# Optimization experiments

Measured on AMD Instinct MI355X. Metric: run time of the kernel, lower is better.

Reference implementation:

```python
import jax, jax.numpy as jnp
import numpy as np

EMB = 1024
HEADS = 16
HEAD_DIM = EMB // HEADS
D_FF = 4 * EMB
EPS = 1e-5


def setup_inputs() -> dict:
    key = jax.random.key(0)
    ks = jax.random.split(key, 12)
    b, t = 4, 2048
    sc = 0.02
    return {
        "x": jax.random.normal(ks[0], (b, t, EMB), dtype=jnp.float32),
        # weights stored [in, out] (transpose of torch Linear.weight)
        "w_attn": jax.random.normal(ks[1], (EMB, 3 * EMB), dtype=jnp.float32) * sc,
        "b_attn": jnp.zeros((3 * EMB,), dtype=jnp.float32),
        "w_proj": jax.random.normal(ks[2], (EMB, EMB), dtype=jnp.float32) * sc,
        "b_proj": jnp.zeros((EMB,), dtype=jnp.float32),
        "ln1_g": jnp.ones((EMB,), dtype=jnp.float32),
        "ln1_b": jnp.zeros((EMB,), dtype=jnp.float32),
        "w_ff1": jax.random.normal(ks[3], (EMB, D_FF), dtype=jnp.float32) * sc,
        "b_ff1": jnp.zeros((D_FF,), dtype=jnp.float32),
        "w_ff2": jax.random.normal(ks[4], (D_FF, EMB), dtype=jnp.float32) * sc,
        "b_ff2": jnp.zeros((EMB,), dtype=jnp.float32),
        "ln2_g": jnp.ones((EMB,), dtype=jnp.float32),
        "ln2_b": jnp.zeros((EMB,), dtype=jnp.float32),
    }


def _layernorm(x, g, b):
    mu = jnp.mean(x, axis=-1, keepdims=True)
    var = jnp.var(x, axis=-1, keepdims=True)
    return (x - mu) * jax.lax.rsqrt(var + EPS) * g + b


def reference(x, w_attn, b_attn, w_proj, b_proj, ln1_g, ln1_b,
              w_ff1, b_ff1, w_ff2, b_ff2, ln2_g, ln2_b):
    b, t, e = x.shape
    h, s = HEADS, HEAD_DIM
    # fused qkv projection (GPT2-style c_attn)
    qkv = x @ w_attn + b_attn                      # [b, t, 3e]
    q, k, v = jnp.split(qkv, 3, axis=-1)
    q = q.reshape(b, t, h, s).transpose(0, 2, 1, 3)  # [b, h, t, s]
    k = k.reshape(b, t, h, s).transpose(0, 2, 1, 3)
    v = v.reshape(b, t, h, s).transpose(0, 2, 1, 3)
    dot = jnp.einsum('bhqs,bhks->bhqk', q, k) / jnp.sqrt(jnp.float32(s))
    # causal mask: mask_(..., mask_diagonal=False) zeroes i < j (strict upper)
    causal = jnp.tril(jnp.ones((t, t), dtype=bool))
    dot = jnp.where(causal, dot, jnp.float32(-jnp.inf))
    att = jax.nn.softmax(dot, axis=-1)
    out = jnp.einsum('bhqk,bhks->bhqs', att, v)    # [b, h, t, s]
    out = out.transpose(0, 2, 1, 3).reshape(b, t, e)
    attended = out @ w_proj + b_proj
    # residual + LayerNorm (dropout is identity in eval mode)
    x1 = _layernorm(attended + x, ln1_g, ln1_b)
    ff = jax.nn.relu(x1 @ w_ff1 + b_ff1) @ w_ff2 + b_ff2
    return _layernorm(ff + x1, ln2_g, ln2_b)
```

## Files before the change

kernel.cpp:

```cpp
#include <hip/hip_runtime.h>
#include <hip/hip_bf16.h>


typedef __attribute__((ext_vector_type(8))) short bf16x8;
typedef __attribute__((ext_vector_type(4))) float f32x4;

__device__ __forceinline__ unsigned short f2b(float f) {
  unsigned int u = __float_as_uint(f);
  u += 0x7fffu + ((u >> 16) & 1u);
  return (unsigned short)(u >> 16);
}
__device__ __forceinline__ unsigned int pk2b(float a, float b) {
  __hip_bfloat162 h = __float22bfloat162_rn(make_float2(a, b));
  return *(unsigned int*)&h;
}
__device__ __forceinline__ void gload_lds16(const unsigned short* g, unsigned short* l) {
  __builtin_amdgcn_global_load_lds((const __attribute__((address_space(1))) void*)g,
                                   (__attribute__((address_space(3))) void*)l, 16, 0, 0);
}

__global__ __launch_bounds__(256) void cvt_bf16(const float* __restrict__ in,
                                                unsigned short* __restrict__ out, long n) {
  long i = ((long)blockIdx.x * 256 + threadIdx.x) * 4;
  if (i >= n) return;
  float4 v = *(const float4*)(in + i);
  *(ushort4*)(out + i) = make_ushort4(f2b(v.x), f2b(v.y), f2b(v.z), f2b(v.w));
}

__global__ __launch_bounds__(256) void transpose_bf16(const float* __restrict__ in,
                                                      unsigned short* __restrict__ out,
                                                      int R, int C) {
  __shared__ float tile[32][33];
  int c0 = blockIdx.x * 32, r0 = blockIdx.y * 32;
  for (int i = threadIdx.y; i < 32; i += 8)
    tile[i][threadIdx.x] = in[(long)(r0 + i) * C + c0 + threadIdx.x];
  __syncthreads();
  for (int i = threadIdx.y; i < 32; i += 8)
    out[(long)(c0 + i) * R + r0 + threadIdx.x] = f2b(tile[threadIdx.x][i]);
}

template <int EPI>
__global__ __launch_bounds__(512, 2) void gemm256(const unsigned short* __restrict__ A,
                                                  const unsigned short* __restrict__ Bt,
                                                  const float* __restrict__ bias,
                                                  void* __restrict__ Cout,
                                                  void* __restrict__ Cout2,
                                                  int N, int K, int Kstride) {
  __shared__ __align__(16) unsigned short As[4][256 * 32];
  __shared__ __align__(16) unsigned short Bs[4][256 * 32];

  int tid = threadIdx.x;
  int wv = tid >> 6, lane = tid & 63, quad = lane >> 4, l16 = lane & 15;
  int wm = wv >> 2, wn = wv & 3;

  int nwg = gridDim.x, id = blockIdx.x;
  int sid = (id & 7) * (nwg >> 3) + (id >> 3);
  int bm256 = (sid & 31) * 256, bn256 = (sid >> 5) * 256;
  int chunk = blockIdx.y;
  long kbase = (long)chunk * K;

  int row1 = tid >> 2, row2 = row1 + 128;
  long dsl = ((tid & 3) ^ ((tid >> 3) & 3)) * 8;
  const unsigned short* Ap1 = A + (long)(bm256 + row1) * Kstride + kbase + dsl;
  const unsigned short* Ap2 = A + (long)(bm256 + row2) * Kstride + kbase + dsl;
  const unsigned short* Bp1 = Bt + (long)(bn256 + row1) * Kstride + kbase + dsl;
  const unsigned short* Bp2 = Bt + (long)(bn256 + row2) * Kstride + kbase + dsl;
  int ldsoff1 = wv * 512, ldsoff2 = wv * 512 + 4096;

  auto stage = [&](int t) {
    int buf = t & 3;
    long ko = (long)t * 32;
    gload_lds16(Ap1 + ko, &As[buf][ldsoff1]);
    gload_lds16(Ap2 + ko, &As[buf][ldsoff2]);
    gload_lds16(Bp1 + ko, &Bs[buf][ldsoff1]);
    gload_lds16(Bp2 + ko, &Bs[buf][ldsoff2]);
  };

  f32x4 acc[8][4] = {};
  int sl8 = (quad ^ ((l16 >> 1) & 3)) * 8;
  int arow = wm * 128 + l16;
  int brow = wn * 64 + l16;

  int NT = K >> 5;
  stage(0); stage(1); stage(2);
  asm volatile("s_waitcnt vmcnt(8)\n\ts_barrier" ::: "memory");
  __builtin_amdgcn_sched_barrier(0);

  for (int t = 0; t < NT; ++t) {
    if (t + 3 < NT) stage(t + 3);
    __builtin_amdgcn_sched_barrier(0);
    const unsigned short* Ab = &As[t & 3][0];
    const unsigned short* Bb = &Bs[t & 3][0];
    bf16x8 af[8], bfr[4];
#pragma unroll
    for (int i = 0; i < 8; ++i)
      af[i] = *(const bf16x8*)(Ab + (arow + i * 16) * 32 + sl8);
#pragma unroll
    for (int j = 0; j < 4; ++j)
      bfr[j] = *(const bf16x8*)(Bb + (brow + j * 16) * 32 + sl8);
    __builtin_amdgcn_s_setprio(1);
#pragma unroll
    for (int i = 0; i < 8; ++i)
#pragma unroll
      for (int j = 0; j < 4; ++j)
        acc[i][j] = __builtin_amdgcn_mfma_f32_16x16x32_bf16(af[i], bfr[j], acc[i][j], 0, 0, 0);
    __builtin_amdgcn_s_setprio(0);
    __builtin_amdgcn_sched_barrier(0);
    if (t + 1 < NT) {
      if (t + 3 < NT)       asm volatile("s_waitcnt vmcnt(8)\n\ts_barrier" ::: "memory");
      else if (t + 3 == NT) asm volatile("s_waitcnt vmcnt(4)\n\ts_barrier" ::: "memory");
      else                  asm volatile("s_waitcnt vmcnt(0)\n\ts_barrier" ::: "memory");
      __builtin_amdgcn_sched_barrier(0);
    }
  }

  void* Cbase = chunk ? Cout2 : Cout;
#pragma unroll
  for (int i = 0; i < 8; ++i) {
#pragma unroll
    for (int j = 0; j < 4; ++j) {
      int gn = bn256 + wn * 64 + j * 16 + l16;
      float bv = chunk ? 0.f : bias[gn];
      if (EPI == 3 && gn >= 2048) {
        int h = (gn >> 6) & 15, s = gn & 63;
        int gm0 = bm256 + wm * 128 + i * 16 + quad * 4;
        int b = gm0 >> 11, tt0 = gm0 & 2047;
        unsigned short* vt = (unsigned short*)Cout + 16777216L;
        ushort4 us;
        us.x = f2b(acc[i][j][0] + bv);
        us.y = f2b(acc[i][j][1] + bv);
        us.z = f2b(acc[i][j][2] + bv);
        us.w = f2b(acc[i][j][3] + bv);
        *(ushort4*)(vt + (((long)(b * 16 + h)) * 64 + s) * 2048 + tt0) = us;
      } else {
#pragma unroll
        for (int r = 0; r < 4; ++r) {
          int gm = bm256 + wm * 128 + i * 16 + quad * 4 + r;
          float v = acc[i][j][r] + bv;
          if (EPI == 2) v = fmaxf(v, 0.f);
          if (EPI == 0) {
            ((float*)Cbase)[(long)gm * N + gn] = v;
          } else if (EPI == 2) {
            ((unsigned short*)Cbase)[(long)gm * N + gn] = f2b(v);
          } else {
            float sc = (gn < 1024) ? 0.18033688011112042f : 1.0f;
            ((unsigned short*)Cbase)[(long)gm * 2048 + gn] = f2b(v * sc);
          }
        }
      }
    }
  }
}

__global__ __launch_bounds__(256) void attn_mfma(const unsigned short* __restrict__ qkv,
                                                 unsigned short* __restrict__ outp) {
  const int LD = 72;
  __shared__ __align__(16) unsigned short Ks[64 * LD];
  __shared__ __align__(16) unsigned short Vts[64 * LD];
  __shared__ __align__(16) unsigned short Ps[4][16 * LD];
  int qa = blockIdx.x, qb = 31 - qa;
  int h = blockIdx.y, b = blockIdx.z;
  int t = threadIdx.x;
  int w = t >> 6, lane = t & 63, quad = lane >> 4, l16 = lane & 15;
  const unsigned short* qg = qkv + (long)(b * 2048) * 2048 + h * 64;
  const unsigned short* kg = qg + 1024;
  const unsigned short* vg = qkv + 16777216L + (((long)(b * 16 + h)) * 64) * 2048;
  unsigned short* Pw = &Ps[w][0];

  bf16x8 qfa[2], qfb[2];
#pragma unroll
  for (int ks = 0; ks < 2; ++ks) {
    qfa[ks] = *(const bf16x8*)(qg + (long)(qa * 64 + w * 16 + l16) * 2048 + ks * 32 + quad * 8);
    qfb[ks] = *(const bf16x8*)(qg + (long)(qb * 64 + w * 16 + l16) * 2048 + ks * 32 + quad * 8);
  }

  int sr = t >> 2, sc = (t & 3) * 16;
  const unsigned short* kp = kg + (long)sr * 2048 + sc;
  const unsigned short* vp = vg + (long)sr * 2048 + sc;
  int4 kv0 = *(const int4*)kp, kv1 = *(const int4*)(kp + 8);
  int4 vv0 = *(const int4*)vp, vv1 = *(const int4*)(vp + 8);
  kp += (long)64 * 2048;
  vp += 64;

  f32x4 oa[4] = {}, ob[4] = {};
  f32x4 la = {}, lb = {};
  const short ONE = 0x3F80;
  bf16x8 ones = {ONE, ONE, ONE, ONE, ONE, ONE, ONE, ONE};

  auto process = [&](const bf16x8* qf, int qt, int kt, f32x4* oacc, f32x4& lacc) {
    bool diag = (kt == qt);
#pragma unroll
    for (int rg = 0; rg < 4; ++rg) {
      bf16x8 kf0 = *(const bf16x8*)(Ks + (rg * 16 + l16) * LD + quad * 8);
      bf16x8 kf1 = *(const bf16x8*)(Ks + (rg * 16 + l16) * LD + 32 + quad * 8);
      f32x4 st = {};
      st = __builtin_amdgcn_mfma_f32_16x16x32_bf16(kf0, qf[0], st, 0, 0, 0);
      st = __builtin_amdgcn_mfma_f32_16x16x32_bf16(kf1, qf[1], st, 0, 0, 0);
      if (diag) {
        int kq = rg * 16 + quad * 4;
        int qq = w * 16 + l16;
#pragma unroll
        for (int r = 0; r < 4; ++r)
          if (kq + r > qq) st[r] = -1e30f;
      }
      unsigned int lo = pk2b(exp2f(st[0]), exp2f(st[1]));
      unsigned int hi = pk2b(exp2f(st[2]), exp2f(st[3]));
      *(uint2*)(Pw + l16 * LD + rg * 16 + quad * 4) = make_uint2(lo, hi);
    }
#pragma unroll
    for (int kc = 0; kc < 2; ++kc) {
      bf16x8 ap = *(const bf16x8*)(Pw + l16 * LD + kc * 32 + quad * 8);
      lacc = __builtin_amdgcn_mfma_f32_16x16x32_bf16(ap, ones, lacc, 0, 0, 0);
#pragma unroll
      for (int sg = 0; sg < 4; ++sg) {
        bf16x8 vf = *(const bf16x8*)(Vts + (sg * 16 + l16) * LD + kc * 32 + quad * 8);
        oacc[sg] = __builtin_amdgcn_mfma_f32_16x16x32_bf16(ap, vf, oacc[sg], 0, 0, 0);
      }
    }
  };

  for (int kt = 0; kt <= qb; ++kt) {
    __syncthreads();
    *(int4*)(Ks + sr * LD + sc) = kv0;
    *(int4*)(Ks + sr * LD + sc + 8) = kv1;
    *(int4*)(Vts + sr * LD + sc) = vv0;
    *(int4*)(Vts + sr * LD + sc + 8) = vv1;
    __syncthreads();
    if (kt < qb) {
      kv0 = *(const int4*)kp; kv1 = *(const int4*)(kp + 8);
      vv0 = *(const int4*)vp; vv1 = *(const int4*)(vp + 8);
      kp += (long)64 * 2048;
      vp += 64;
    }
    process(qfb, qb, kt, ob, lb);
    if (kt <= qa) process(qfa, qa, kt, oa, la);
  }

  auto epi = [&](int qt, f32x4* oacc, f32x4& lacc) {
#pragma unroll
    for (int r = 0; r < 4; ++r) {
      float invl = 1.f / lacc[r];
      int row = qt * 64 + w * 16 + quad * 4 + r;
      unsigned short* op = outp + ((long)(b * 2048 + row)) * 1024 + h * 64;
#pragma unroll
      for (int sg = 0; sg < 4; ++sg) op[sg * 16 + l16] = f2b(oacc[sg][r] * invl);
    }
  };
  epi(qa, oa, la);
  epi(qb, ob, lb);
}

__global__ __launch_bounds__(256) void ln_kernel(const float* __restrict__ a,
                                                 const float* __restrict__ a2,
                                                 const float* __restrict__ res,
                                                 const float* __restrict__ gam,
                                                 const float* __restrict__ bet,
                                                 float* __restrict__ outf,
                                                 unsigned short* __restrict__ outb) {
  int row = blockIdx.x, t = threadIdx.x;
  float4 av = *(const float4*)(a + (long)row * 1024 + t * 4);
  float4 rv = *(const float4*)(res + (long)row * 1024 + t * 4);
  float v0 = av.x + rv.x, v1 = av.y + rv.y, v2 = av.z + rv.z, v3 = av.w + rv.w;
  if (a2) {
    float4 a2v = *(const float4*)(a2 + (long)row * 1024 + t * 4);
    v0 += a2v.x; v1 += a2v.y; v2 += a2v.z; v3 += a2v.w;
  }
  float s = v0 + v1 + v2 + v3;
  float ss = v0 * v0 + v1 * v1 + v2 * v2 + v3 * v3;
#pragma unroll
  for (int off = 32; off >= 1; off >>= 1) {
    s += __shfl_down(s, off);
    ss += __shfl_down(ss, off);
  }
  __shared__ float sb[4], ssb[4];
  __shared__ float mean_s, inv_s;
  int w = t >> 6, lane = t & 63;
  if (lane == 0) { sb[w] = s; ssb[w] = ss; }
  __syncthreads();
  if (t == 0) {
    float S = sb[0] + sb[1] + sb[2] + sb[3];
    float SS = ssb[0] + ssb[1] + ssb[2] + ssb[3];
    float mean = S * (1.f / 1024.f);
    float var = SS * (1.f / 1024.f) - mean * mean;
    mean_s = mean;
    inv_s = rsqrtf(var + 1e-5f);
  }
  __syncthreads();
  float mean = mean_s, inv = inv_s;
  int c = t * 4;
  float4 gv = *(const float4*)(gam + c);
  float4 bv = *(const float4*)(bet + c);
  float y0 = (v0 - mean) * inv * gv.x + bv.x;
  float y1 = (v1 - mean) * inv * gv.y + bv.y;
  float y2 = (v2 - mean) * inv * gv.z + bv.z;
  float y3 = (v3 - mean) * inv * gv.w + bv.w;
  *(float4*)(outf + (long)row * 1024 + c) = make_float4(y0, y1, y2, y3);
  if (outb) {
    *(ushort4*)(outb + (long)row * 1024 + c) = make_ushort4(f2b(y0), f2b(y1), f2b(y2), f2b(y3));
  }
}

extern "C" void kernel_launch(void* const* d_in, const int* in_sizes, int n_in,
                              void* d_out, int out_size, void* d_ws, size_t ws_size,
                              hipStream_t stream) {
  const float* x      = (const float*)d_in[0];
  const float* w_attn = (const float*)d_in[1];
  const float* b_attn = (const float*)d_in[2];
  const float* w_proj = (const float*)d_in[3];
  const float* b_proj = (const float*)d_in[4];
  const float* ln1_g  = (const float*)d_in[5];
  const float* ln1_b  = (const float*)d_in[6];
  const float* w_ff1  = (const float*)d_in[7];
  const float* b_ff1  = (const float*)d_in[8];
  const float* w_ff2  = (const float*)d_in[9];
  const float* b_ff2  = (const float*)d_in[10];
  const float* ln2_g  = (const float*)d_in[11];
  const float* ln2_b  = (const float*)d_in[12];

  const long M = 8192, E = 1024;
  char* ws = (char*)d_ws;
  unsigned short* xb   = (unsigned short*)ws; ws += M * E * 2;
  unsigned short* wTa  = (unsigned short*)ws; ws += 3072L * 1024 * 2;
  unsigned short* wTp  = (unsigned short*)ws; ws += 1024L * 1024 * 2;
  unsigned short* wTf1 = (unsigned short*)ws; ws += 4096L * 1024 * 2;
  unsigned short* wTf2 = (unsigned short*)ws; ws += 4096L * 1024 * 2;
  unsigned short* qkvb = (unsigned short*)ws; ws += M * 3072 * 2;
  unsigned short* attb = (unsigned short*)ws; ws += M * E * 2;
  float* a1f = (float*)ws; ws += M * E * 4;
  float* x1f = (float*)ws; ws += M * E * 4;
  unsigned short* x1b = (unsigned short*)ws; ws += M * E * 2;
  unsigned short* hb = qkvb;
  float* f2 = a1f;
  float* prj1 = (float*)qkvb;
  float* ff21 = (float*)d_ws;

  cvt_bf16<<<dim3((M * E) / 4 / 256), dim3(256), 0, stream>>>(x, xb, M * E);
  transpose_bf16<<<dim3(3072 / 32, 1024 / 32), dim3(32, 8), 0, stream>>>(w_attn, wTa, 1024, 3072);
  transpose_bf16<<<dim3(1024 / 32, 1024 / 32), dim3(32, 8), 0, stream>>>(w_proj, wTp, 1024, 1024);
  transpose_bf16<<<dim3(4096 / 32, 1024 / 32), dim3(32, 8), 0, stream>>>(w_ff1, wTf1, 1024, 4096);
  transpose_bf16<<<dim3(1024 / 32, 4096 / 32), dim3(32, 8), 0, stream>>>(w_ff2, wTf2, 4096, 1024);
  gemm256<3><<<dim3(384, 1), dim3(512), 0, stream>>>(xb, wTa, b_attn, qkvb, nullptr, 3072, 1024, 1024);
  attn_mfma<<<dim3(16, 16, 4), dim3(256), 0, stream>>>(qkvb, attb);
  gemm256<0><<<dim3(128, 2), dim3(512), 0, stream>>>(attb, wTp, b_proj, a1f, prj1, 1024, 512, 1024);
  ln_kernel<<<dim3(8192), dim3(256), 0, stream>>>(a1f, prj1, x, ln1_g, ln1_b, x1f, x1b);
  gemm256<2><<<dim3(512, 1), dim3(512), 0, stream>>>(x1b, wTf1, b_ff1, hb, nullptr, 4096, 1024, 1024);
  gemm256<0><<<dim3(128, 2), dim3(512), 0, stream>>>(hb, wTf2, b_ff2, f2, ff21, 1024, 2048, 4096);
  ln_kernel<<<dim3(8192), dim3(256), 0, stream>>>(f2, ff21, x1f, ln2_g, ln2_b, (float*)d_out, nullptr);
}
```

Baseline: 602.0 us.

## Split GEMM k-step into two half-phases interleaving A/B prefetch with MFMA

```diff
diff --git a/kernel.cpp b/kernel.cpp
--- a/kernel.cpp
+++ b/kernel.cpp
@@ -65,16 +65,7 @@
   const unsigned short* Ap2 = A + (long)(bm256 + row2) * Kstride + kbase + dsl;
   const unsigned short* Bp1 = Bt + (long)(bn256 + row1) * Kstride + kbase + dsl;
   const unsigned short* Bp2 = Bt + (long)(bn256 + row2) * Kstride + kbase + dsl;
-  int ldsoff1 = wv * 512, ldsoff2 = wv * 512 + 4096;
-
-  auto stage = [&](int t) {
-    int buf = t & 3;
-    long ko = (long)t * 32;
-    gload_lds16(Ap1 + ko, &As[buf][ldsoff1]);
-    gload_lds16(Ap2 + ko, &As[buf][ldsoff2]);
-    gload_lds16(Bp1 + ko, &Bs[buf][ldsoff1]);
-    gload_lds16(Bp2 + ko, &Bs[buf][ldsoff2]);
-  };
+  int lo1 = wv * 512, lo2 = wv * 512 + 4096;
 
   f32x4 acc[8][4] = {};
   int sl8 = (quad ^ ((l16 >> 1) & 3)) * 8;
@@ -82,36 +73,68 @@
   int brow = wn * 64 + l16;
 
   int NT = K >> 5;
-  stage(0); stage(1); stage(2);
-  asm volatile("s_waitcnt vmcnt(8)\n\ts_barrier" ::: "memory");
+  gload_lds16(Ap1, &As[0][lo1]); gload_lds16(Ap2, &As[0][lo2]);
+  gload_lds16(Bp1, &Bs[0][lo1]); gload_lds16(Bp2, &Bs[0][lo2]);
+  gload_lds16(Ap1 + 32, &As[1][lo1]); gload_lds16(Ap2 + 32, &As[1][lo2]);
+  gload_lds16(Bp1 + 32, &Bs[1][lo1]); gload_lds16(Bp2 + 32, &Bs[1][lo2]);
+  gload_lds16(Ap1 + 64, &As[2][lo1]); gload_lds16(Ap2 + 64, &As[2][lo2]);
+  asm volatile("s_waitcnt vmcnt(6)\n\ts_barrier" ::: "memory");
   __builtin_amdgcn_sched_barrier(0);
 
-  for (int t = 0; t < NT; ++t) {
-    if (t + 3 < NT) stage(t + 3);
-    __builtin_amdgcn_sched_barrier(0);
-    const unsigned short* Ab = &As[t & 3][0];
-    const unsigned short* Bb = &Bs[t & 3][0];
-    bf16x8 af[8], bfr[4];
-#pragma unroll
-    for (int i = 0; i < 8; ++i)
+  for (int tau = 0; tau < NT; ++tau) {
+    const unsigned short* Ab = &As[tau & 3][0];
+    const unsigned short* Bb = &Bs[tau & 3][0];
+    bf16x8 af[4], bfr[4];
+#pragma unroll
+    for (int i = 0; i < 4; ++i)
       af[i] = *(const bf16x8*)(Ab + (arow + i * 16) * 32 + sl8);
 #pragma unroll
     for (int j = 0; j < 4; ++j)
       bfr[j] = *(const bf16x8*)(Bb + (brow + j * 16) * 32 + sl8);
+    if (tau + 2 < NT) {
+      long ko = (long)(tau + 2) * 32;
+      int s = (tau + 2) & 3;
+      gload_lds16(Bp1 + ko, &Bs[s][lo1]);
+      gload_lds16(Bp2 + ko, &Bs[s][lo2]);
+    }
+    asm volatile("s_barrier\n\ts_waitcnt lgkmcnt(0)" ::: "memory");
+    __builtin_amdgcn_sched_barrier(0);
     __builtin_amdgcn_s_setprio(1);
 #pragma unroll
-    for (int i = 0; i < 8; ++i)
+    for (int i = 0; i < 4; ++i)
 #pragma unroll
       for (int j = 0; j < 4; ++j)
         acc[i][j] = __builtin_amdgcn_mfma_f32_16x16x32_bf16(af[i], bfr[j], acc[i][j], 0, 0, 0);
     __builtin_amdgcn_s_setprio(0);
+    __builtin_amdgcn_s_barrier();
     __builtin_amdgcn_sched_barrier(0);
-    if (t + 1 < NT) {
-      if (t + 3 < NT)       asm volatile("s_waitcnt vmcnt(8)\n\ts_barrier" ::: "memory");
-      else if (t + 3 == NT) asm volatile("s_waitcnt vmcnt(4)\n\ts_barrier" ::: "memory");
-      else                  asm volatile("s_waitcnt vmcnt(0)\n\ts_barrier" ::: "memory");
-      __builtin_amdgcn_sched_barrier(0);
-    }
+    bf16x8 ag[4];
+#pragma unroll
+    for (int i = 0; i < 4; ++i)
+      ag[i] = *(const bf16x8*)(Ab + (arow + (i + 4) * 16) * 32 + sl8);
+    if (tau + 3 < NT) {
+      long ko = (long)(tau + 3) * 32;
+      int s = (tau + 3) & 3;
+      gload_lds16(Ap1 + ko, &As[s][lo1]);
+      gload_lds16(Ap2 + ko, &As[s][lo2]);
+    }
+    asm volatile("s_barrier\n\ts_waitcnt lgkmcnt(0)" ::: "memory");
+    __builtin_amdgcn_sched_barrier(0);
+    __builtin_amdgcn_s_setprio(1);
+#pragma unroll
+    for (int i = 0; i < 4; ++i)
+#pragma unroll
+      for (int j = 0; j < 4; ++j)
+        acc[i + 4][j] = __builtin_amdgcn_mfma_f32_16x16x32_bf16(ag[i], bfr[j], acc[i + 4][j], 0, 0, 0);
+    __builtin_amdgcn_s_setprio(0);
+    if (tau + 3 < NT) {
+      asm volatile("s_waitcnt vmcnt(6)\n\ts_barrier" ::: "memory");
+    } else if (tau + 2 < NT) {
+      asm volatile("s_waitcnt vmcnt(4)\n\ts_barrier" ::: "memory");
+    } else if (tau + 1 < NT) {
+      asm volatile("s_waitcnt vmcnt(0)\n\ts_barrier" ::: "memory");
+    }
+    __builtin_amdgcn_sched_barrier(0);
   }
 
   void* Cbase = chunk ? Cout2 : Cout;
```

Result: faster. 567.1 us (-5.8%).
